# Optimization experiments

Hardware: AMD Instinct MI355X
Metric: run time of the kernel (lower is better)

The kernel has to match this reference:

```python
import jax, jax.numpy as jnp
import numpy as np

DIM = 1024
N_HEADS = 16
HEAD_DIM = DIM // N_HEADS
ROPE_BASE = 10000.0


def setup_inputs() -> dict:
    key = jax.random.key(0)
    ks = jax.random.split(key, 5)
    B, T = 4, 2048
    s_in = 1.0 / np.sqrt(DIM)
    x = jax.random.normal(ks[0], (B, T, DIM), dtype=jnp.float32)
    W_qkv = jax.random.uniform(ks[1], (DIM, 3 * DIM), jnp.float32, -s_in, s_in)
    b_qkv = jax.random.uniform(ks[2], (3 * DIM,), jnp.float32, -s_in, s_in)
    W_proj = jax.random.uniform(ks[3], (DIM, DIM), jnp.float32, -s_in, s_in)
    b_proj = jax.random.uniform(ks[4], (DIM,), jnp.float32, -s_in, s_in)
    return {"x": x, "W_qkv": W_qkv, "b_qkv": b_qkv, "W_proj": W_proj, "b_proj": b_proj}


def _rope_cos_sin(T, dtype):
    inv_freq = 1.0 / (ROPE_BASE ** (jnp.arange(0, HEAD_DIM, 2, dtype=jnp.float32) / HEAD_DIM))
    t = jnp.arange(T, dtype=jnp.float32)
    freqs = jnp.outer(t, inv_freq)            # (T, HEAD_DIM/2)
    emb = jnp.concatenate([freqs, freqs], -1)  # (T, HEAD_DIM)
    return jnp.cos(emb).astype(dtype), jnp.sin(emb).astype(dtype)


def _rotate_half(x):
    x1, x2 = jnp.split(x, 2, axis=-1)
    return jnp.concatenate([-x2, x1], axis=-1)


def reference(x, W_qkv, b_qkv, W_proj, b_proj):
    B, T, C = x.shape
    qkv = x @ W_qkv + b_qkv                              # (B, T, 3C)
    qkv = qkv.reshape(B, T, 3, N_HEADS, HEAD_DIM)
    qkv = jnp.transpose(qkv, (2, 0, 3, 1, 4))            # (3, B, H, T, d)
    q, k, v = qkv[0], qkv[1], qkv[2]
    cos, sin = _rope_cos_sin(T, x.dtype)
    cos = cos[None, None]                                # (1,1,T,d)
    sin = sin[None, None]
    q = q * cos + _rotate_half(q) * sin
    k = k * cos + _rotate_half(k) * sin
    scale = 1.0 / np.sqrt(HEAD_DIM)
    scores = jnp.einsum('bhqd,bhkd->bhqk', q, k) * scale  # (B,H,T,T)
    attn = jax.nn.softmax(scores, axis=-1)
    out = jnp.einsum('bhqk,bhkd->bhqd', attn, v)          # (B,H,T,d)
    out = jnp.transpose(out, (0, 2, 1, 3)).reshape(B, T, C)
    return out @ W_proj + b_proj
```

## Files before the change

kernel.cpp:

```cpp
#include <hip/hip_runtime.h>
#include <hip/hip_bf16.h>
#include <cstdint>
#include <cstddef>

typedef __bf16 bf16x8 __attribute__((ext_vector_type(8)));
typedef float f32x4 __attribute__((ext_vector_type(4)));
typedef float f32x16 __attribute__((ext_vector_type(16)));
typedef unsigned short ushort8 __attribute__((ext_vector_type(8)));

#define MFMA16(a, b, c) __builtin_amdgcn_mfma_f32_16x16x32_bf16(a, b, c, 0, 0, 0)
#define MFMA32(a, b, c) __builtin_amdgcn_mfma_f32_32x32x16_bf16(a, b, c, 0, 0, 0)

__device__ __forceinline__ void gll16(const void* g, void* l) {
  __builtin_amdgcn_global_load_lds((__attribute__((address_space(1))) unsigned int*)g,
                                   (__attribute__((address_space(3))) unsigned int*)l,
                                   16, 0, 0);
}

__device__ __forceinline__ float exp2_raw(float x) {
  return __builtin_amdgcn_exp2f(x);
}

__device__ __forceinline__ bf16x8 pack8(float a0, float a1, float a2, float a3,
                                        float a4, float a5, float a6, float a7) {
  unsigned w0, w1, w2, w3;
  asm("v_cvt_pk_bf16_f32 %0, %1, %2" : "=v"(w0) : "v"(a0), "v"(a1));
  asm("v_cvt_pk_bf16_f32 %0, %1, %2" : "=v"(w1) : "v"(a2), "v"(a3));
  asm("v_cvt_pk_bf16_f32 %0, %1, %2" : "=v"(w2) : "v"(a4), "v"(a5));
  asm("v_cvt_pk_bf16_f32 %0, %1, %2" : "=v"(w3) : "v"(a6), "v"(a7));
  asm("v_permlane32_swap_b32 %0, %1" : "+v"(w0), "+v"(w2));
  asm("v_permlane32_swap_b32 %0, %1" : "+v"(w1), "+v"(w3));
  union { unsigned u[4]; bf16x8 v; } r;
  r.u[0] = w0; r.u[1] = w1; r.u[2] = w2; r.u[3] = w3;
  return r.v;
}


__global__ void cvt_x(const float* __restrict__ in, __bf16* __restrict__ out,
                      float2* __restrict__ tab) {
  int i = (blockIdx.x * 256 + threadIdx.x) * 8;
  float4 a = *(const float4*)(in + i);
  float4 c = *(const float4*)(in + i + 4);
  bf16x8 r;
  r[0] = (__bf16)a.x; r[1] = (__bf16)a.y; r[2] = (__bf16)a.z; r[3] = (__bf16)a.w;
  r[4] = (__bf16)c.x; r[5] = (__bf16)c.y; r[6] = (__bf16)c.z; r[7] = (__bf16)c.w;
  *(bf16x8*)(out + i) = r;
  if (blockIdx.x < 256) {
    int idx = blockIdx.x * 256 + threadIdx.x;
    int t = idx >> 5, ii = idx & 31;
    float invf = exp2f(-(float)ii * (13.287712379549449f / 32.0f));
    float ang = (float)t * invf;
    tab[idx] = make_float2(cosf(ang), sinf(ang));
  }
}

__global__ void transp_w(const float* __restrict__ Wq, __bf16* __restrict__ Wtq,
                         const float* __restrict__ Wp, __bf16* __restrict__ Wtp) {
  __shared__ float tile[32][33];
  int bx = blockIdx.x;
  const float* W; __bf16* Wt; int N;
  if (bx < 96) { W = Wq; Wt = Wtq; N = 3072; }
  else         { W = Wp; Wt = Wtp; N = 1024; bx -= 96; }
  const int K = 1024;
  int n0 = bx * 32, k0 = blockIdx.y * 32;
  int tx = threadIdx.x & 31, ty = threadIdx.x >> 5;
  #pragma unroll
  for (int r = ty; r < 32; r += 8)
    tile[r][tx] = W[(size_t)(k0 + r) * N + n0 + tx];
  __syncthreads();
  #pragma unroll
  for (int r = ty; r < 32; r += 8)
    Wt[(size_t)(n0 + r) * K + k0 + tx] = (__bf16)tile[tx][r];
}

template <int EPI>
__global__ __launch_bounds__(256, 3) void gemm_bt(
    const __bf16* __restrict__ A, const __bf16* __restrict__ Bt,
    const float* __restrict__ bias, float* __restrict__ Cf,
    __bf16* __restrict__ qp, __bf16* __restrict__ kp, __bf16* __restrict__ vtp,
    const float2* __restrict__ ctab, int M, int N, int K) {
  __shared__ __align__(16) char smem[49152];
  const int tid = threadIdx.x;
  const int w = tid >> 6, l = tid & 63, l15 = l & 15, g = l >> 4;
  const int wr = w >> 1, wc = w & 1;
  const int brow = blockIdx.y * 128, bcol = blockIdx.x * 128;

  f32x4 acc[4][4] = {};
  const int rsub = tid >> 3;
  const int sf   = (rsub & 7) ^ (((rsub >> 3) & 3) << 1);
  const int schunk = (((tid & 7) ^ sf) << 4);
  const int fr0 = (l15 & 7) ^ (((l15 >> 3) & 3) << 1);
  const int fr1 = (l15 & 7) ^ ((((l15 >> 3) + 2) & 3) << 1);

  for (int kt = 0; kt < K; kt += 64) {
    __syncthreads();
    #pragma unroll
    for (int i = 0; i < 4; ++i) {
      const char* ga = (const char*)(A + (size_t)(brow + i * 32 + rsub) * K + kt) + schunk;
      gll16(ga, smem + i * 4096 + tid * 16);
      const char* gb = (const char*)(Bt + (size_t)(bcol + i * 32 + rsub) * K + kt) + schunk;
      gll16(gb, smem + 16384 + i * 4096 + tid * 16);
    }
    __syncthreads();
    #pragma unroll
    for (int kk = 0; kk < 2; ++kk) {
      bf16x8 af[4], bfr[4];
      #pragma unroll
      for (int m = 0; m < 4; ++m) {
        int fx = (m & 1) ? fr1 : fr0;
        af[m] = *(const bf16x8*)(smem + (wr * 64 + m * 16 + l15) * 128 +
                                 (((kk * 4 + g) ^ fx) << 4));
      }
      #pragma unroll
      for (int n = 0; n < 4; ++n) {
        int fx = (n & 1) ? fr1 : fr0;
        bfr[n] = *(const bf16x8*)(smem + 16384 + (wc * 64 + n * 16 + l15) * 128 +
                                  (((kk * 4 + g) ^ fx) << 4));
      }
      __builtin_amdgcn_s_setprio(1);
      #pragma unroll
      for (int m = 0; m < 4; ++m)
        #pragma unroll
        for (int n = 0; n < 4; ++n)
          acc[m][n] = MFMA16(af[m], bfr[n], acc[m][n]);
      __builtin_amdgcn_s_setprio(0);
    }
  }

  const int colb = bcol + wc * 64;
  float bs[4];
  #pragma unroll
  for (int n = 0; n < 4; ++n) bs[n] = bias[colb + n * 16 + l15];

  if (EPI == 1) {
    #pragma unroll
    for (int m = 0; m < 4; ++m)
      #pragma unroll
      for (int j = 0; j < 4; ++j) {
        int row = brow + wr * 64 + m * 16 + g * 4 + j;
        float* crow = Cf + (size_t)row * N + colb;
        #pragma unroll
        for (int n = 0; n < 4; ++n)
          crow[n * 16 + l15] = acc[m][n][j] + bs[n];
      }
  } else {
    const int which = colb >> 10;
    if (which < 2) {
      const int h = (colb & 1023) >> 6;
      __bf16* dst = (which == 0) ? qp : kp;
      const float SCLQ = 0.18033688011112042f;
      #pragma unroll
      for (int m = 0; m < 4; ++m)
        #pragma unroll
        for (int j = 0; j < 4; ++j) {
          int row = brow + wr * 64 + m * 16 + g * 4 + j;
          int bb = row >> 11, t = row & 2047;
          float v0 = acc[m][0][j] + bs[0];
          float v1 = acc[m][1][j] + bs[1];
          float v2 = acc[m][2][j] + bs[2];
          float v3 = acc[m][3][j] + bs[3];
          float2 cs0 = ctab[t * 32 + l15];
          float2 cs1 = ctab[t * 32 + 16 + l15];
          float r0 = v0 * cs0.x - v2 * cs0.y;
          float r2 = v2 * cs0.x + v0 * cs0.y;
          float r1 = v1 * cs1.x - v3 * cs1.y;
          float r3 = v3 * cs1.x + v1 * cs1.y;
          v0 = r0; v1 = r1; v2 = r2; v3 = r3;
          if (which == 0) { v0 *= SCLQ; v1 *= SCLQ; v2 *= SCLQ; v3 *= SCLQ; }
          __bf16* orow = dst + ((size_t)(bb * 16 + h) * 2048 + t) * 64;
          orow[l15]      = (__bf16)v0;
          orow[16 + l15] = (__bf16)v1;
          orow[32 + l15] = (__bf16)v2;
          orow[48 + l15] = (__bf16)v3;
        }
    } else {
      __syncthreads();
      #pragma unroll
      for (int n = 0; n < 4; ++n) {
        int cloc = wc * 64 + n * 16 + l15;
        char* cbase = smem + cloc * 256;
        int sw = (cloc & 15) << 4;
        #pragma unroll
        for (int m = 0; m < 4; ++m)
          #pragma unroll
          for (int j = 0; j < 4; ++j) {
            int rloc = wr * 64 + m * 16 + g * 4 + j;
            *(__bf16*)(cbase + ((rloc * 2) ^ sw)) = (__bf16)(acc[m][n][j] + bs[n]);
          }
      }
      __syncthreads();
      const int b = brow >> 11, t0 = brow & 2047;
      const int h0 = (bcol - 2048) >> 6;
      const int tch = l & 15;
      #pragma unroll
      for (int i = 0; i < 8; ++i) {
        int c = w * 32 + i * 4 + (l >> 4);
        ushort8 vrow = *(const ushort8*)(smem + c * 256 + ((tch * 16) ^ ((c & 15) << 4)));
        __bf16* dst = vtp + ((size_t)((b * 16 + h0 + (c >> 6)) * 64 + (c & 63)) * 2048 +
                             t0 + tch * 8);
        *(ushort8*)dst = vrow;
      }
    }
  }
}

__global__ __launch_bounds__(256, 2) void flash_attn(
    const __bf16* __restrict__ q, const __bf16* __restrict__ k,
    const __bf16* __restrict__ vt, __bf16* __restrict__ o) {
  __shared__ __align__(16) char smem[32768];
  const int id = blockIdx.x;
  const int nid = (id & 7) * 64 + (id >> 3);
  const int bh = nid >> 3, qb = nid & 7;
  const int b = bh >> 4, h = bh & 15;
  const int tid = threadIdx.x, w = tid >> 6, l = tid & 63;
  const int l31 = l & 31, hi = l >> 5;

  const char* kbase  = (const char*)(k  + (size_t)bh * 2048 * 64);
  const char* vtbase = (const char*)(vt + (size_t)bh * 64 * 2048);

  bf16x8 qfa[4], qfb[4];
  const int qrow0a = qb * 256 + w * 32;
  const int qrow0b = qrow0a + 128;
  #pragma unroll
  for (int ks = 0; ks < 4; ++ks) {
    qfa[ks] = *(const bf16x8*)(q + (size_t)bh * 2048 * 64 +
                               (size_t)(qrow0a + l31) * 64 + ks * 16 + hi * 8);
    qfb[ks] = *(const bf16x8*)(q + (size_t)bh * 2048 * 64 +
                               (size_t)(qrow0b + l31) * 64 + ks * 16 + hi * 8);
  }

  f32x16 accA[2] = {}, accB[2] = {};
  float lra = 0.f, lrb = 0.f;

  const int koff[2] = { 0, 16384 };
  const int voff[2] = { 8192, 24576 };

  const int srow = tid >> 3;
  const int ssw  = (((tid & 7) ^ ((tid >> 3) & 7) ^ (((tid >> 6) & 3) << 1)) << 4);
  const int swz  = (((l & 7) ^ (((l >> 3) & 3) << 1)) << 4);

  gll16(kbase + srow * 128 + ssw,                  smem + koff[0] + tid * 16);
  gll16(kbase + (srow + 32) * 128 + ssw,           smem + koff[0] + 4096 + tid * 16);
  gll16(vtbase + (size_t)srow * 4096 + ssw,        smem + voff[0] + tid * 16);
  gll16(vtbase + (size_t)(srow + 32) * 4096 + ssw, smem + voff[0] + 4096 + tid * 16);
  __syncthreads();

  for (int t = 0; t < 32; ++t) {
    const int cur = t & 1;
    char* Kc = smem + koff[cur];
    char* Vc = smem + voff[cur];
    if (t < 31) {
      char* Kn = smem + koff[cur ^ 1];
      char* Vn = smem + voff[cur ^ 1];
      const char* gk = kbase + (size_t)(t + 1) * 8192;
      gll16(gk + srow * 128 + ssw,        Kn + tid * 16);
      gll16(gk + (srow + 32) * 128 + ssw, Kn + 4096 + tid * 16);
      const char* gv = vtbase + (size_t)(t + 1) * 128;
      gll16(gv + (size_t)srow * 4096 + ssw,        Vn + tid * 16);
      gll16(gv + (size_t)(srow + 32) * 4096 + ssw, Vn + 4096 + tid * 16);
    }

    f32x16 sa0 = {}, sa1 = {}, sb0 = {}, sb1 = {};
    __builtin_amdgcn_s_setprio(1);
    #pragma unroll
    for (int ks = 0; ks < 4; ++ks) {
      bf16x8 kf0 = *(const bf16x8*)(Kc + (l31) * 128 + ((ks * 32 + hi * 16) ^ swz));
      bf16x8 kf1 = *(const bf16x8*)(Kc + (32 + l31) * 128 + ((ks * 32 + hi * 16) ^ swz));
      sa0 = MFMA32(kf0, qfa[ks], sa0);
      sa1 = MFMA32(kf1, qfa[ks], sa1);
      sb0 = MFMA32(kf0, qfb[ks], sb0);
      sb1 = MFMA32(kf1, qfb[ks], sb1);
    }
    __builtin_amdgcn_s_setprio(0);

    bf16x8 paa[4];
    {
      float p[16];
      #pragma unroll
      for (int r = 0; r < 16; ++r) p[r] = exp2_raw(sa0[r]);
      lra += (((p[0] + p[1]) + (p[2] + p[3])) + ((p[4] + p[5]) + (p[6] + p[7]))) +
             (((p[8] + p[9]) + (p[10] + p[11])) + ((p[12] + p[13]) + (p[14] + p[15])));
      paa[0] = pack8(p[0], p[1], p[2], p[3], p[4], p[5], p[6], p[7]);
      paa[1] = pack8(p[8], p[9], p[10], p[11], p[12], p[13], p[14], p[15]);
    }
    {
      float p[16];
      #pragma unroll
      for (int r = 0; r < 16; ++r) p[r] = exp2_raw(sa1[r]);
      lra += (((p[0] + p[1]) + (p[2] + p[3])) + ((p[4] + p[5]) + (p[6] + p[7]))) +
             (((p[8] + p[9]) + (p[10] + p[11])) + ((p[12] + p[13]) + (p[14] + p[15])));
      paa[2] = pack8(p[0], p[1], p[2], p[3], p[4], p[5], p[6], p[7]);
      paa[3] = pack8(p[8], p[9], p[10], p[11], p[12], p[13], p[14], p[15]);
    }

    bf16x8 vf0[4], vf1[4];
    __builtin_amdgcn_s_setprio(1);
    #pragma unroll
    for (int ks = 0; ks < 4; ++ks) {
      vf0[ks] = *(const bf16x8*)(Vc + (l31) * 128 + ((ks * 32 + hi * 16) ^ swz));
      vf1[ks] = *(const bf16x8*)(Vc + (32 + l31) * 128 + ((ks * 32 + hi * 16) ^ swz));
      accA[0] = MFMA32(paa[ks], vf0[ks], accA[0]);
      accA[1] = MFMA32(paa[ks], vf1[ks], accA[1]);
    }
    __builtin_amdgcn_s_setprio(0);

    bf16x8 pab[4];
    {
      float p[16];
      #pragma unroll
      for (int r = 0; r < 16; ++r) p[r] = exp2_raw(sb0[r]);
      lrb += (((p[0] + p[1]) + (p[2] + p[3])) + ((p[4] + p[5]) + (p[6] + p[7]))) +
             (((p[8] + p[9]) + (p[10] + p[11])) + ((p[12] + p[13]) + (p[14] + p[15])));
      pab[0] = pack8(p[0], p[1], p[2], p[3], p[4], p[5], p[6], p[7]);
      pab[1] = pack8(p[8], p[9], p[10], p[11], p[12], p[13], p[14], p[15]);
    }
    {
      float p[16];
      #pragma unroll
      for (int r = 0; r < 16; ++r) p[r] = exp2_raw(sb1[r]);
      lrb += (((p[0] + p[1]) + (p[2] + p[3])) + ((p[4] + p[5]) + (p[6] + p[7]))) +
             (((p[8] + p[9]) + (p[10] + p[11])) + ((p[12] + p[13]) + (p[14] + p[15])));
      pab[2] = pack8(p[0], p[1], p[2], p[3], p[4], p[5], p[6], p[7]);
      pab[3] = pack8(p[8], p[9], p[10], p[11], p[12], p[13], p[14], p[15]);
    }

    __builtin_amdgcn_s_setprio(1);
    #pragma unroll
    for (int ks = 0; ks < 4; ++ks) {
      accB[0] = MFMA32(pab[ks], vf0[ks], accB[0]);
      accB[1] = MFMA32(pab[ks], vf1[ks], accB[1]);
    }
    __builtin_amdgcn_s_setprio(0);
    __syncthreads();
  }

  float lrfa = lra + __shfl_xor(lra, 32);
  float lrfb = lrb + __shfl_xor(lrb, 32);
  __bf16* obase = o + (size_t)(b * 2048) * 1024 + h * 64;
  #pragma unroll
  for (int r = 0; r < 16; ++r) {
    int qloc = (r & 3) + 8 * (r >> 2) + 4 * hi;
    float inva = 1.0f / __shfl(lrfa, qloc);
    float invb = 1.0f / __shfl(lrfb, qloc);
    __bf16* orowa = obase + (size_t)(qrow0a + qloc) * 1024;
    __bf16* orowb = obase + (size_t)(qrow0b + qloc) * 1024;
    orowa[l31]      = (__bf16)(accA[0][r] * inva);
    orowa[32 + l31] = (__bf16)(accA[1][r] * inva);
    orowb[l31]      = (__bf16)(accB[0][r] * invb);
    orowb[32 + l31] = (__bf16)(accB[1][r] * invb);
  }
}


extern "C" void kernel_launch(void* const* d_in, const int* in_sizes, int n_in,
                              void* d_out, int out_size, void* d_ws, size_t ws_size,
                              hipStream_t stream) {
  const float* x     = (const float*)d_in[0];
  const float* Wqkv  = (const float*)d_in[1];
  const float* bqkv  = (const float*)d_in[2];
  const float* Wproj = (const float*)d_in[3];
  const float* bproj = (const float*)d_in[4];
  float* out = (float*)d_out;

  char* ws = (char*)d_ws;
  __bf16* xb  = (__bf16*)(ws);
  __bf16* wtq = (__bf16*)(ws + 16777216);
  __bf16* wtp = (__bf16*)(ws + 23068672);
  __bf16* qp  = (__bf16*)(ws + 25165824);
  __bf16* kp  = (__bf16*)(ws + 41943040);
  __bf16* vtp = (__bf16*)(ws + 58720256);
  __bf16* ao  = (__bf16*)(ws + 75497472);
  float2* ct  = (float2*)(ws + 92274688);
  if (ws_size < 92798976) return;

  cvt_x<<<4096, 256, 0, stream>>>(x, xb, ct);
  transp_w<<<dim3(128, 32), 256, 0, stream>>>(Wqkv, wtq, Wproj, wtp);
  gemm_bt<0><<<dim3(24, 64), 256, 0, stream>>>(xb, wtq, bqkv, nullptr, qp, kp, vtp, ct,
                                               8192, 3072, 1024);
  flash_attn<<<512, 256, 0, stream>>>(qp, kp, vtp, ao);
  gemm_bt<1><<<dim3(8, 64), 256, 0, stream>>>(ao, wtp, bproj, out, nullptr, nullptr,
                                              nullptr, nullptr, 8192, 1024, 1024);
}
```

Before: 169.8 us.

## Triple-buffer K/V tiles in flash attention with explicit vmcnt waits

Result: no change. 171.4 us (+1.0%).

```diff
diff --git a/kernel.cpp b/kernel.cpp
--- a/kernel.cpp
+++ b/kernel.cpp
@@ -207,7 +207,7 @@
 __global__ __launch_bounds__(256, 2) void flash_attn(
     const __bf16* __restrict__ q, const __bf16* __restrict__ k,
     const __bf16* __restrict__ vt, __bf16* __restrict__ o) {
-  __shared__ __align__(16) char smem[32768];
+  __shared__ __align__(16) char smem[49152];
   const int id = blockIdx.x;
   const int nid = (id & 7) * 64 + (id >> 3);
   const int bh = nid >> 3, qb = nid & 7;
@@ -232,33 +232,34 @@
   f32x16 accA[2] = {}, accB[2] = {};
   float lra = 0.f, lrb = 0.f;
 
-  const int koff[2] = { 0, 16384 };
-  const int voff[2] = { 8192, 24576 };
-
   const int srow = tid >> 3;
   const int ssw  = (((tid & 7) ^ ((tid >> 3) & 7) ^ (((tid >> 6) & 3) << 1)) << 4);
   const int swz  = (((l & 7) ^ (((l >> 3) & 3) << 1)) << 4);
 
-  gll16(kbase + srow * 128 + ssw,                  smem + koff[0] + tid * 16);
-  gll16(kbase + (srow + 32) * 128 + ssw,           smem + koff[0] + 4096 + tid * 16);
-  gll16(vtbase + (size_t)srow * 4096 + ssw,        smem + voff[0] + tid * 16);
-  gll16(vtbase + (size_t)(srow + 32) * 4096 + ssw, smem + voff[0] + 4096 + tid * 16);
-  __syncthreads();
+#define STAGE_KV(tile, buf) do {                                             \
+    char* Kn = smem + (buf) * 16384;                                         \
+    char* Vn = Kn + 8192;                                                    \
+    const char* gk = kbase + (size_t)(tile) * 8192;                          \
+    gll16(gk + srow * 128 + ssw,        Kn + tid * 16);                      \
+    gll16(gk + (srow + 32) * 128 + ssw, Kn + 4096 + tid * 16);               \
+    const char* gv = vtbase + (size_t)(tile) * 128;                          \
+    gll16(gv + (size_t)srow * 4096 + ssw,        Vn + tid * 16);             \
+    gll16(gv + (size_t)(srow + 32) * 4096 + ssw, Vn + 4096 + tid * 16);      \
+  } while (0)
+
+  STAGE_KV(0, 0);
+  STAGE_KV(1, 1);
 
   for (int t = 0; t < 32; ++t) {
-    const int cur = t & 1;
-    char* Kc = smem + koff[cur];
-    char* Vc = smem + voff[cur];
-    if (t < 31) {
-      char* Kn = smem + koff[cur ^ 1];
-      char* Vn = smem + voff[cur ^ 1];
-      const char* gk = kbase + (size_t)(t + 1) * 8192;
-      gll16(gk + srow * 128 + ssw,        Kn + tid * 16);
-      gll16(gk + (srow + 32) * 128 + ssw, Kn + 4096 + tid * 16);
-      const char* gv = vtbase + (size_t)(t + 1) * 128;
-      gll16(gv + (size_t)srow * 4096 + ssw,        Vn + tid * 16);
-      gll16(gv + (size_t)(srow + 32) * 4096 + ssw, Vn + 4096 + tid * 16);
-    }
+    if (t < 30) STAGE_KV(t + 2, (t + 2) % 3);
+    if (t < 30)       asm volatile("s_waitcnt vmcnt(8)" ::: "memory");
+    else if (t == 30) asm volatile("s_waitcnt vmcnt(4)" ::: "memory");
+    else              asm volatile("s_waitcnt vmcnt(0)" ::: "memory");
+    __builtin_amdgcn_s_barrier();
+    asm volatile("" ::: "memory");
+
+    char* Kc = smem + (t % 3) * 16384;
+    char* Vc = Kc + 8192;
 
     f32x16 sa0 = {}, sa1 = {}, sb0 = {}, sb1 = {};
     __builtin_amdgcn_s_setprio(1);
@@ -331,8 +332,12 @@
       accB[1] = MFMA32(pab[ks], vf1[ks], accB[1]);
     }
     __builtin_amdgcn_s_setprio(0);
-    __syncthreads();
-  }
+
+    asm volatile("" ::: "memory");
+    __builtin_amdgcn_s_barrier();
+    asm volatile("" ::: "memory");
+  }
+#undef STAGE_KV
 
   float lrfa = lra + __shfl_xor(lra, 32);
   float lrfb = lrb + __shfl_xor(lrb, 32);
```
